# Optimization experiments

Measured on AMD Instinct MI355X. Metric: run time of the kernel, lower is better.

Reference implementation:

```python
import jax, jax.numpy as jnp
import numpy as np

REMOVE_FACTOR = 1000000.0


def setup_inputs() -> dict:
    key = jax.random.key(0)
    ks = jax.random.split(key, 6)
    B, Te, Td = 4, 512, 128
    D_en, D_de, U = 256, 512, 128
    en_seq = jax.random.normal(ks[0], (B, Te, D_en), dtype=jnp.float32)
    de_seq = jax.random.normal(ks[1], (B, Td, D_de), dtype=jnp.float32)
    mask = jax.random.randint(ks[2], (B, Te), 0, 2).astype(jnp.int32)
    w_en = jax.random.normal(ks[3], (D_en, U), dtype=jnp.float32) * (1.0 / np.sqrt(D_en))
    w_de = jax.random.normal(ks[4], (D_de, U), dtype=jnp.float32) * (1.0 / np.sqrt(D_de))
    nu = jax.random.normal(ks[5], (U, 1), dtype=jnp.float32) * (1.0 / np.sqrt(U))
    return {"en_seq": en_seq, "de_seq": de_seq, "mask": mask,
            "w_en": w_en, "w_de": w_de, "nu": nu}


def reference(en_seq, de_seq, mask, w_en, w_de, nu):
    # en_seq: [B,Te,D_en], de_seq: [B,Td,D_de], mask: [B,Te] (0/1)
    m = mask.astype(en_seq.dtype)
    en = en_seq * m[..., None]                         # masked encoder states
    en_p = jnp.einsum('bte,eu->btu', en, w_en)          # [B,Te,U]
    de_p = jnp.einsum('bdf,fu->bdu', de_seq, w_de)      # [B,Td,U]
    # additive (Bahdanau) scores: scores[b,td,te] = tanh(en_p[te]+de_p[td]) @ nu
    h = jnp.tanh(en_p[:, None, :, :] + de_p[:, :, None, :])  # [B,Td,Te,U]
    mu = jnp.einsum('bdtu,u->bdt', h, nu[:, 0])               # [B,Td,Te]
    mu = mu + (m[:, None, :] - 1.0) * REMOVE_FACTOR           # mask bias
    alphas = jax.nn.softmax(mu, axis=-1)                      # softmax over Te
    sum_en = jnp.einsum('bdt,btc->bdc', alphas, en)           # [B,Td,D_en]
    return jnp.concatenate([de_seq, sum_en], axis=-1)         # [B,Td,D_de+D_en]
```

## Files before the change

### kernel.cpp

```cpp
#include <hip/hip_runtime.h>

namespace {
constexpr int B = 4, Te = 512, Td = 128, Den = 256, Dde = 512, U = 128;
constexpr float REMOVE = 1000000.0f;
constexpr float L2E2 = 2.885390081777927f;

__device__ __forceinline__ unsigned short f2bf(float f) {
  unsigned u = __float_as_uint(f);
  u += 0x7FFFu + ((u >> 16) & 1u);
  return (unsigned short)(u >> 16);
}
__device__ __forceinline__ float bf2f(unsigned short h) {
  return __uint_as_float(((unsigned)h) << 16);
}
__device__ __forceinline__ void tanh_fma(float ep, float dv, float nv, float& acc) {
  float e = __builtin_amdgcn_exp2f((ep + dv) * L2E2);
  float r = __builtin_amdgcn_rcpf(e + 1.0f);
  acc = fmaf(fmaf(-2.0f, r, 1.0f), nv, acc);
}
__device__ __forceinline__ void fma4(const float4& w, float x, float* a) {
  a[0] = fmaf(x, w.x, a[0]); a[1] = fmaf(x, w.y, a[1]);
  a[2] = fmaf(x, w.z, a[2]); a[3] = fmaf(x, w.w, a[3]);
}

__global__ __launch_bounds__(512) void proj_kernel(
    const float* __restrict__ en_seq, const float* __restrict__ de_seq,
    const int* __restrict__ mask, const float* __restrict__ w_en,
    const float* __restrict__ w_de, unsigned short* __restrict__ en_pT,
    unsigned short* __restrict__ en_bf, float* __restrict__ de_pA,
    float* __restrict__ de_pB, float* __restrict__ out) {
  __shared__ float xs[4096];
  const int blk = blockIdx.x, tid = threadIdx.x;

  if (blk < 128) {
    const int r0 = blk * 16;
    for (int i = tid; i < 1024; i += 512) {
      int row = i >> 6, c4 = i & 63;
      float m = (float)mask[r0 + row];
      float4 v = *(const float4*)(en_seq + (size_t)(r0 + row) * Den + c4 * 4);
      v.x *= m; v.y *= m; v.z *= m; v.w *= m;
      *(float4*)(xs + row * 256 + c4 * 4) = v;
      ushort4 h; h.x = f2bf(v.x); h.y = f2bf(v.y); h.z = f2bf(v.z); h.w = f2bf(v.w);
      *(ushort4*)(en_bf + (size_t)(r0 + row) * Den + c4 * 4) = h;
    }
    __syncthreads();
    const int rg = tid >> 5, ug = tid & 31, u0 = ug * 4;
    float acc[4] = {0, 0, 0, 0};
    for (int k = 0; k < 256; k += 4) {
      const float* wp = w_en + (size_t)k * U + u0;
      float4 w0 = *(const float4*)(wp);
      float4 w1 = *(const float4*)(wp + U);
      float4 w2 = *(const float4*)(wp + 2 * U);
      float4 w3 = *(const float4*)(wp + 3 * U);
      float4 xv = *(const float4*)(xs + rg * 256 + k);
      fma4(w0, xv.x, acc); fma4(w1, xv.y, acc);
      fma4(w2, xv.z, acc); fma4(w3, xv.w, acc);
    }
    __syncthreads();
#pragma unroll
    for (int j = 0; j < 4; ++j) xs[(u0 + j) * 17 + rg] = acc[j];
    __syncthreads();
    {
      int u = tid >> 2, q = tid & 3;
      const float* p = xs + u * 17 + q * 4;
      ushort4 h; h.x = f2bf(p[0]); h.y = f2bf(p[1]); h.z = f2bf(p[2]); h.w = f2bf(p[3]);
      int b = r0 >> 9, teb = (r0 & 511) + q * 4;
      *(ushort4*)(en_pT + ((size_t)b * U + u) * Te + teb) = h;
    }
  } else {
    const int q = blk - 128, rt = q >> 1, kh = q & 1;
    const int r0 = rt * 8, k0 = kh * 256;
    {
      int row = tid >> 6, c4 = tid & 63;
      float4 v = *(const float4*)(de_seq + (size_t)(r0 + row) * Dde + k0 + c4 * 4);
      *(float4*)(xs + row * 256 + c4 * 4) = v;
      *(float4*)(out + (size_t)(r0 + row) * 768 + k0 + c4 * 4) = v;
    }
    __syncthreads();
    const int ks = tid >> 8, rg = (tid >> 5) & 7, ug = tid & 31, u0 = ug * 4;
    float acc[4] = {0, 0, 0, 0};
    for (int k = ks * 128; k < ks * 128 + 128; k += 4) {
      const float* wp = w_de + (size_t)(k0 + k) * U + u0;
      float4 w0 = *(const float4*)(wp);
      float4 w1 = *(const float4*)(wp + U);
      float4 w2 = *(const float4*)(wp + 2 * U);
      float4 w3 = *(const float4*)(wp + 3 * U);
      float4 xv = *(const float4*)(xs + rg * 256 + k);
      fma4(w0, xv.x, acc); fma4(w1, xv.y, acc);
      fma4(w2, xv.z, acc); fma4(w3, xv.w, acc);
    }
    __syncthreads();
    *(float4*)(xs + (ks * 8 + rg) * 128 + u0) =
        make_float4(acc[0], acc[1], acc[2], acc[3]);
    __syncthreads();
    float* dst = kh ? de_pB : de_pA;
    for (int i = tid; i < 1024; i += 512) {
      int r = i >> 7, u = i & 127;
      dst[(size_t)(r0 + r) * U + u] = xs[r * 128 + u] + xs[(8 + r) * 128 + u];
    }
  }
}

__global__ __launch_bounds__(512) void attn_kernel(
    const unsigned short* __restrict__ en_pT, const unsigned short* __restrict__ en_bf,
    const float* __restrict__ de_pA, const float* __restrict__ de_pB,
    const float* __restrict__ nu, const int* __restrict__ mask,
    float* __restrict__ out) {
  __shared__ float dep[256];
  __shared__ float nus[128];
  __shared__ float mbs[512];
  __shared__ float als[1024];
  __shared__ float scr[4096];
  const int blk = blockIdx.x, tid = threadIdx.x;
  const int b = blk >> 6, tp = blk & 63;
  const int gtd0 = b * Td + tp * 2;

  mbs[tid] = ((float)mask[b * Te + tid] - 1.0f) * REMOVE;
  if (tid < 64) {
    int r = tid >> 5, q = tid & 31;
    float4 a = *(const float4*)(de_pA + (size_t)(gtd0 + r) * U + q * 4);
    float4 c = *(const float4*)(de_pB + (size_t)(gtd0 + r) * U + q * 4);
    *(float4*)(dep + r * 128 + q * 4) =
        make_float4(a.x + c.x, a.y + c.y, a.z + c.z, a.w + c.w);
  } else if (tid < 96) {
    int q2 = tid - 64;
    *(float4*)(nus + q2 * 4) = *(const float4*)(nu + q2 * 4);
  }
  __syncthreads();

  {
    const int ts = tid & 127, uq = tid >> 7;
    const int te0 = ts * 4;
    float s0[4] = {0, 0, 0, 0}, s1[4] = {0, 0, 0, 0};
    const unsigned short* ep = en_pT + (size_t)b * U * Te;
#pragma unroll 4
    for (int u = uq * 32; u < uq * 32 + 32; ++u) {
      ushort4 h = *(const ushort4*)(ep + (size_t)u * Te + te0);
      float dv0 = dep[u], dv1 = dep[128 + u], nv = nus[u];
      float e0 = bf2f(h.x), e1 = bf2f(h.y), e2 = bf2f(h.z), e3 = bf2f(h.w);
      tanh_fma(e0, dv0, nv, s0[0]); tanh_fma(e0, dv1, nv, s1[0]);
      tanh_fma(e1, dv0, nv, s0[1]); tanh_fma(e1, dv1, nv, s1[1]);
      tanh_fma(e2, dv0, nv, s0[2]); tanh_fma(e2, dv1, nv, s1[2]);
      tanh_fma(e3, dv0, nv, s0[3]); tanh_fma(e3, dv1, nv, s1[3]);
    }
    *(float4*)(scr + (uq * 2 + 0) * 512 + te0) = make_float4(s0[0], s0[1], s0[2], s0[3]);
    *(float4*)(scr + (uq * 2 + 1) * 512 + te0) = make_float4(s1[0], s1[1], s1[2], s1[3]);
  }
  __syncthreads();

  {
    const int wid = tid >> 6, lane = tid & 63;
    if (wid < 2) {
      float v[8]; float mx = -3.0e38f;
#pragma unroll
      for (int i = 0; i < 8; ++i) {
        int te = lane + i * 64;
        float s = scr[(0 + wid) * 512 + te] + scr[(2 + wid) * 512 + te] +
                  scr[(4 + wid) * 512 + te] + scr[(6 + wid) * 512 + te] + mbs[te];
        v[i] = s; mx = fmaxf(mx, s);
      }
#pragma unroll
      for (int o = 32; o >= 1; o >>= 1) mx = fmaxf(mx, __shfl_xor(mx, o));
      float ssum = 0.f;
#pragma unroll
      for (int i = 0; i < 8; ++i) { v[i] = __expf(v[i] - mx); ssum += v[i]; }
#pragma unroll
      for (int o = 32; o >= 1; o >>= 1) ssum += __shfl_xor(ssum, o);
      float inv = 1.0f / ssum;
#pragma unroll
      for (int i = 0; i < 8; ++i) als[(lane + i * 64) * 2 + wid] = v[i] * inv;
    }
  }
  __syncthreads();

  {
    const int wid = tid >> 6, lane = tid & 63;
    const int ch0 = lane * 4;
    const unsigned short* eb = en_bf + (size_t)b * Te * Den;
    float p0[4] = {0, 0, 0, 0}, p1[4] = {0, 0, 0, 0};
#pragma unroll 4
    for (int t = 0; t < 64; ++t) {
      int te = wid * 64 + t;
      ushort4 h = *(const ushort4*)(eb + (size_t)te * Den + ch0);
      float2 al = *(const float2*)(als + te * 2);
      float e0 = bf2f(h.x), e1 = bf2f(h.y), e2 = bf2f(h.z), e3 = bf2f(h.w);
      p0[0] = fmaf(al.x, e0, p0[0]); p0[1] = fmaf(al.x, e1, p0[1]);
      p0[2] = fmaf(al.x, e2, p0[2]); p0[3] = fmaf(al.x, e3, p0[3]);
      p1[0] = fmaf(al.y, e0, p1[0]); p1[1] = fmaf(al.y, e1, p1[1]);
      p1[2] = fmaf(al.y, e2, p1[2]); p1[3] = fmaf(al.y, e3, p1[3]);
    }
    *(float4*)(scr + (wid * 2 + 0) * 256 + ch0) = make_float4(p0[0], p0[1], p0[2], p0[3]);
    *(float4*)(scr + (wid * 2 + 1) * 256 + ch0) = make_float4(p1[0], p1[1], p1[2], p1[3]);
  }
  __syncthreads();

  {
    int td = tid >> 8, ch = tid & 255;
    float v = 0.f;
#pragma unroll
    for (int w = 0; w < 8; ++w) v += scr[(w * 2 + td) * 256 + ch];
    out[(size_t)(gtd0 + td) * 768 + 512 + ch] = v;
  }
}
}

extern "C" void kernel_launch(void* const* d_in, const int* in_sizes, int n_in,
                              void* d_out, int out_size, void* d_ws, size_t ws_size,
                              hipStream_t stream) {
  const float* en_seq = (const float*)d_in[0];
  const float* de_seq = (const float*)d_in[1];
  const int*   mask   = (const int*)d_in[2];
  const float* w_en   = (const float*)d_in[3];
  const float* w_de   = (const float*)d_in[4];
  const float* nu     = (const float*)d_in[5];
  float* out = (float*)d_out;

  unsigned short* en_pT = (unsigned short*)d_ws;
  unsigned short* en_bf = en_pT + (size_t)B * U * Te;
  float* de_pA = (float*)(en_bf + (size_t)B * Te * Den);
  float* de_pB = de_pA + (size_t)B * Td * U;

  hipLaunchKernelGGL(proj_kernel, dim3(256), dim3(512), 0, stream,
                     en_seq, de_seq, mask, w_en, w_de, en_pT, en_bf,
                     de_pA, de_pB, out);
  hipLaunchKernelGGL(attn_kernel, dim3(256), dim3(512), 0, stream,
                     en_pT, en_bf, de_pA, de_pB, nu, mask, out);
}
```

Baseline: 41.12 us.

## Repartition both kernels into smaller 256-thread blocks with one decoder row per block

Both kernels move from 512-thread to 256-thread blocks with more blocks each. The attention kernel now handles one decoder timestep per block instead of two, so the 64x8 softmax layout becomes a block-wide reduction through shared-memory warp partials. The projection kernel halves its rows per block and drops the split-K reduction through shared memory. The aim is more blocks to fill the CUs and less shared memory per block, but each en_pT and en_bf tile is now reread once per decoder row instead of shared across two, roughly doubling that traffic.

Measured after the change: 42.65 us. 1.04x slower.

```diff
diff --git a/kernel.cpp b/kernel.cpp
--- a/kernel.cpp
+++ b/kernel.cpp
@@ -23,18 +23,18 @@
   a[2] = fmaf(x, w.z, a[2]); a[3] = fmaf(x, w.w, a[3]);
 }
 
-__global__ __launch_bounds__(512) void proj_kernel(
+__global__ __launch_bounds__(256) void proj_kernel(
     const float* __restrict__ en_seq, const float* __restrict__ de_seq,
     const int* __restrict__ mask, const float* __restrict__ w_en,
     const float* __restrict__ w_de, unsigned short* __restrict__ en_pT,
     unsigned short* __restrict__ en_bf, float* __restrict__ de_pA,
     float* __restrict__ de_pB, float* __restrict__ out) {
-  __shared__ float xs[4096];
+  __shared__ float xs[2048];
   const int blk = blockIdx.x, tid = threadIdx.x;
 
-  if (blk < 128) {
-    const int r0 = blk * 16;
-    for (int i = tid; i < 1024; i += 512) {
+  if (blk < 256) {
+    const int r0 = blk * 8;
+    for (int i = tid; i < 512; i += 256) {
       int row = i >> 6, c4 = i & 63;
       float m = (float)mask[r0 + row];
       float4 v = *(const float4*)(en_seq + (size_t)(r0 + row) * Den + c4 * 4);
@@ -46,6 +46,7 @@
     __syncthreads();
     const int rg = tid >> 5, ug = tid & 31, u0 = ug * 4;
     float acc[4] = {0, 0, 0, 0};
+#pragma unroll 4
     for (int k = 0; k < 256; k += 4) {
       const float* wp = w_en + (size_t)k * U + u0;
       float4 w0 = *(const float4*)(wp);
@@ -57,29 +58,34 @@
       fma4(w2, xv.z, acc); fma4(w3, xv.w, acc);
     }
     __syncthreads();
-#pragma unroll
-    for (int j = 0; j < 4; ++j) xs[(u0 + j) * 17 + rg] = acc[j];
-    __syncthreads();
-    {
-      int u = tid >> 2, q = tid & 3;
-      const float* p = xs + u * 17 + q * 4;
-      ushort4 h; h.x = f2bf(p[0]); h.y = f2bf(p[1]); h.z = f2bf(p[2]); h.w = f2bf(p[3]);
-      int b = r0 >> 9, teb = (r0 & 511) + q * 4;
-      *(ushort4*)(en_pT + ((size_t)b * U + u) * Te + teb) = h;
+    *(float4*)(xs + rg * 128 + u0) = make_float4(acc[0], acc[1], acc[2], acc[3]);
+    __syncthreads();
+    if (tid < 128) {
+      int u = tid;
+      int b = r0 >> 9, te0 = r0 & 511;
+      ushort4 h0, h1;
+      h0.x = f2bf(xs[0 * 128 + u]); h0.y = f2bf(xs[1 * 128 + u]);
+      h0.z = f2bf(xs[2 * 128 + u]); h0.w = f2bf(xs[3 * 128 + u]);
+      h1.x = f2bf(xs[4 * 128 + u]); h1.y = f2bf(xs[5 * 128 + u]);
+      h1.z = f2bf(xs[6 * 128 + u]); h1.w = f2bf(xs[7 * 128 + u]);
+      unsigned short* dst = en_pT + ((size_t)b * U + u) * Te + te0;
+      *(ushort4*)(dst) = h0;
+      *(ushort4*)(dst + 4) = h1;
     }
   } else {
-    const int q = blk - 128, rt = q >> 1, kh = q & 1;
+    const int q = blk - 256, rt = q >> 1, kh = q & 1;
     const int r0 = rt * 8, k0 = kh * 256;
-    {
-      int row = tid >> 6, c4 = tid & 63;
+    for (int i = tid; i < 512; i += 256) {
+      int row = i >> 6, c4 = i & 63;
       float4 v = *(const float4*)(de_seq + (size_t)(r0 + row) * Dde + k0 + c4 * 4);
       *(float4*)(xs + row * 256 + c4 * 4) = v;
       *(float4*)(out + (size_t)(r0 + row) * 768 + k0 + c4 * 4) = v;
     }
     __syncthreads();
-    const int ks = tid >> 8, rg = (tid >> 5) & 7, ug = tid & 31, u0 = ug * 4;
+    const int rg = tid >> 5, ug = tid & 31, u0 = ug * 4;
     float acc[4] = {0, 0, 0, 0};
-    for (int k = ks * 128; k < ks * 128 + 128; k += 4) {
+#pragma unroll 4
+    for (int k = 0; k < 256; k += 4) {
       const float* wp = w_de + (size_t)(k0 + k) * U + u0;
       float4 w0 = *(const float4*)(wp);
       float4 w1 = *(const float4*)(wp + U);
@@ -89,41 +95,32 @@
       fma4(w0, xv.x, acc); fma4(w1, xv.y, acc);
       fma4(w2, xv.z, acc); fma4(w3, xv.w, acc);
     }
-    __syncthreads();
-    *(float4*)(xs + (ks * 8 + rg) * 128 + u0) =
+    float* dst = kh ? de_pB : de_pA;
+    *(float4*)(dst + (size_t)(r0 + rg) * U + u0) =
         make_float4(acc[0], acc[1], acc[2], acc[3]);
-    __syncthreads();
-    float* dst = kh ? de_pB : de_pA;
-    for (int i = tid; i < 1024; i += 512) {
-      int r = i >> 7, u = i & 127;
-      dst[(size_t)(r0 + r) * U + u] = xs[r * 128 + u] + xs[(8 + r) * 128 + u];
-    }
-  }
-}
-
-__global__ __launch_bounds__(512) void attn_kernel(
+  }
+}
+
+__global__ __launch_bounds__(256) void attn_kernel(
     const unsigned short* __restrict__ en_pT, const unsigned short* __restrict__ en_bf,
     const float* __restrict__ de_pA, const float* __restrict__ de_pB,
     const float* __restrict__ nu, const int* __restrict__ mask,
     float* __restrict__ out) {
-  __shared__ float dep[256];
-  __shared__ float nus[128];
-  __shared__ float mbs[512];
-  __shared__ float als[1024];
-  __shared__ float scr[4096];
+  __shared__ float dep[128], nus[128], mbs[512], als[512];
+  __shared__ float scr[1024];
+  __shared__ float wredA[4], wredB[4];
   const int blk = blockIdx.x, tid = threadIdx.x;
-  const int b = blk >> 6, tp = blk & 63;
-  const int gtd0 = b * Td + tp * 2;
-
-  mbs[tid] = ((float)mask[b * Te + tid] - 1.0f) * REMOVE;
-  if (tid < 64) {
-    int r = tid >> 5, q = tid & 31;
-    float4 a = *(const float4*)(de_pA + (size_t)(gtd0 + r) * U + q * 4);
-    float4 c = *(const float4*)(de_pB + (size_t)(gtd0 + r) * U + q * 4);
-    *(float4*)(dep + r * 128 + q * 4) =
+  const int b = blk >> 7, gtd = blk;
+
+  mbs[tid]       = ((float)mask[b * Te + tid] - 1.0f) * REMOVE;
+  mbs[tid + 256] = ((float)mask[b * Te + tid + 256] - 1.0f) * REMOVE;
+  if (tid < 32) {
+    float4 a = *(const float4*)(de_pA + (size_t)gtd * U + tid * 4);
+    float4 c = *(const float4*)(de_pB + (size_t)gtd * U + tid * 4);
+    *(float4*)(dep + tid * 4) =
         make_float4(a.x + c.x, a.y + c.y, a.z + c.z, a.w + c.w);
-  } else if (tid < 96) {
-    int q2 = tid - 64;
+  } else if (tid < 64) {
+    int q2 = tid - 32;
     *(float4*)(nus + q2 * 4) = *(const float4*)(nu + q2 * 4);
   }
   __syncthreads();
@@ -131,76 +128,62 @@
   {
     const int ts = tid & 127, uq = tid >> 7;
     const int te0 = ts * 4;
-    float s0[4] = {0, 0, 0, 0}, s1[4] = {0, 0, 0, 0};
     const unsigned short* ep = en_pT + (size_t)b * U * Te;
-#pragma unroll 4
-    for (int u = uq * 32; u < uq * 32 + 32; ++u) {
+    float s[4] = {0, 0, 0, 0};
+#pragma unroll 8
+    for (int u = uq * 64; u < uq * 64 + 64; ++u) {
       ushort4 h = *(const ushort4*)(ep + (size_t)u * Te + te0);
-      float dv0 = dep[u], dv1 = dep[128 + u], nv = nus[u];
-      float e0 = bf2f(h.x), e1 = bf2f(h.y), e2 = bf2f(h.z), e3 = bf2f(h.w);
-      tanh_fma(e0, dv0, nv, s0[0]); tanh_fma(e0, dv1, nv, s1[0]);
-      tanh_fma(e1, dv0, nv, s0[1]); tanh_fma(e1, dv1, nv, s1[1]);
-      tanh_fma(e2, dv0, nv, s0[2]); tanh_fma(e2, dv1, nv, s1[2]);
-      tanh_fma(e3, dv0, nv, s0[3]); tanh_fma(e3, dv1, nv, s1[3]);
-    }
-    *(float4*)(scr + (uq * 2 + 0) * 512 + te0) = make_float4(s0[0], s0[1], s0[2], s0[3]);
-    *(float4*)(scr + (uq * 2 + 1) * 512 + te0) = make_float4(s1[0], s1[1], s1[2], s1[3]);
+      float dv = dep[u], nv = nus[u];
+      tanh_fma(bf2f(h.x), dv, nv, s[0]);
+      tanh_fma(bf2f(h.y), dv, nv, s[1]);
+      tanh_fma(bf2f(h.z), dv, nv, s[2]);
+      tanh_fma(bf2f(h.w), dv, nv, s[3]);
+    }
+    *(float4*)(scr + uq * 512 + te0) = make_float4(s[0], s[1], s[2], s[3]);
   }
   __syncthreads();
 
   {
-    const int wid = tid >> 6, lane = tid & 63;
-    if (wid < 2) {
-      float v[8]; float mx = -3.0e38f;
+    const int wid = tid >> 6;
+    float v0 = scr[tid] + scr[512 + tid] + mbs[tid];
+    float v1 = scr[tid + 256] + scr[512 + tid + 256] + mbs[tid + 256];
+    float mx = fmaxf(v0, v1);
 #pragma unroll
-      for (int i = 0; i < 8; ++i) {
-        int te = lane + i * 64;
-        float s = scr[(0 + wid) * 512 + te] + scr[(2 + wid) * 512 + te] +
-                  scr[(4 + wid) * 512 + te] + scr[(6 + wid) * 512 + te] + mbs[te];
-        v[i] = s; mx = fmaxf(mx, s);
-      }
+    for (int o = 32; o >= 1; o >>= 1) mx = fmaxf(mx, __shfl_xor(mx, o));
+    if ((tid & 63) == 0) wredA[wid] = mx;
+    __syncthreads();
+    float bm = fmaxf(fmaxf(wredA[0], wredA[1]), fmaxf(wredA[2], wredA[3]));
+    float e0 = __expf(v0 - bm), e1 = __expf(v1 - bm);
+    float ss = e0 + e1;
 #pragma unroll
-      for (int o = 32; o >= 1; o >>= 1) mx = fmaxf(mx, __shfl_xor(mx, o));
-      float ssum = 0.f;
-#pragma unroll
-      for (int i = 0; i < 8; ++i) { v[i] = __expf(v[i] - mx); ssum += v[i]; }
-#pragma unroll
-      for (int o = 32; o >= 1; o >>= 1) ssum += __shfl_xor(ssum, o);
-      float inv = 1.0f / ssum;
-#pragma unroll
-      for (int i = 0; i < 8; ++i) als[(lane + i * 64) * 2 + wid] = v[i] * inv;
-    }
+    for (int o = 32; o >= 1; o >>= 1) ss += __shfl_xor(ss, o);
+    if ((tid & 63) == 0) wredB[wid] = ss;
+    __syncthreads();
+    float inv = 1.0f / (wredB[0] + wredB[1] + wredB[2] + wredB[3]);
+    als[tid] = e0 * inv;
+    als[tid + 256] = e1 * inv;
   }
   __syncthreads();
 
   {
-    const int wid = tid >> 6, lane = tid & 63;
-    const int ch0 = lane * 4;
+    const int cq = tid & 63, teq = tid >> 6;
+    const int c0 = cq * 4;
     const unsigned short* eb = en_bf + (size_t)b * Te * Den;
-    float p0[4] = {0, 0, 0, 0}, p1[4] = {0, 0, 0, 0};
-#pragma unroll 4
-    for (int t = 0; t < 64; ++t) {
-      int te = wid * 64 + t;
-      ushort4 h = *(const ushort4*)(eb + (size_t)te * Den + ch0);
-      float2 al = *(const float2*)(als + te * 2);
-      float e0 = bf2f(h.x), e1 = bf2f(h.y), e2 = bf2f(h.z), e3 = bf2f(h.w);
-      p0[0] = fmaf(al.x, e0, p0[0]); p0[1] = fmaf(al.x, e1, p0[1]);
-      p0[2] = fmaf(al.x, e2, p0[2]); p0[3] = fmaf(al.x, e3, p0[3]);
-      p1[0] = fmaf(al.y, e0, p1[0]); p1[1] = fmaf(al.y, e1, p1[1]);
-      p1[2] = fmaf(al.y, e2, p1[2]); p1[3] = fmaf(al.y, e3, p1[3]);
-    }
-    *(float4*)(scr + (wid * 2 + 0) * 256 + ch0) = make_float4(p0[0], p0[1], p0[2], p0[3]);
-    *(float4*)(scr + (wid * 2 + 1) * 256 + ch0) = make_float4(p1[0], p1[1], p1[2], p1[3]);
-  }
-  __syncthreads();
-
-  {
-    int td = tid >> 8, ch = tid & 255;
-    float v = 0.f;
-#pragma unroll
-    for (int w = 0; w < 8; ++w) v += scr[(w * 2 + td) * 256 + ch];
-    out[(size_t)(gtd0 + td) * 768 + 512 + ch] = v;
-  }
+    float p[4] = {0, 0, 0, 0};
+#pragma unroll 8
+    for (int t = 0; t < 128; ++t) {
+      int te = teq * 128 + t;
+      ushort4 h = *(const ushort4*)(eb + (size_t)te * Den + c0);
+      float al = als[te];
+      p[0] = fmaf(al, bf2f(h.x), p[0]); p[1] = fmaf(al, bf2f(h.y), p[1]);
+      p[2] = fmaf(al, bf2f(h.z), p[2]); p[3] = fmaf(al, bf2f(h.w), p[3]);
+    }
+    *(float4*)(scr + teq * 256 + c0) = make_float4(p[0], p[1], p[2], p[3]);
+  }
+  __syncthreads();
+
+  out[(size_t)gtd * 768 + 512 + tid] =
+      scr[tid] + scr[256 + tid] + scr[512 + tid] + scr[768 + tid];
 }
 }
 
@@ -220,9 +203,9 @@
   float* de_pA = (float*)(en_bf + (size_t)B * Te * Den);
   float* de_pB = de_pA + (size_t)B * Td * U;
 
-  hipLaunchKernelGGL(proj_kernel, dim3(256), dim3(512), 0, stream,
+  hipLaunchKernelGGL(proj_kernel, dim3(384), dim3(256), 0, stream,
                      en_seq, de_seq, mask, w_en, w_de, en_pT, en_bf,
                      de_pA, de_pB, out);
-  hipLaunchKernelGGL(attn_kernel, dim3(256), dim3(512), 0, stream,
+  hipLaunchKernelGGL(attn_kernel, dim3(512), dim3(256), 0, stream,
                      en_pT, en_bf, de_pA, de_pB, nu, mask, out);
 }
```

## Split attention into score and output kernels with tiled LDS score computation

Applied to the files above, without the earlier changes.

Replaces the fused attention kernel with a score kernel and a separate softmax/weighted-sum kernel. The score kernel stages a 64×128 tile of en_p into swizzled LDS and computes 8 decoder rows per block across 512 blocks. Scores go to a global mu buffer. en_p is stored row-major in te-tiles instead of transposed. The projection kernel is retuned to 256 threads with wider per-thread accumulators. This aims to raise parallelism and reuse in the tanh-heavy score phase, at the cost of an extra launch and a global round trip for the scores.

Result: no change. 41.01 us (-0.3%).

```diff
diff --git a/kernel.cpp b/kernel.cpp
--- a/kernel.cpp
+++ b/kernel.cpp
@@ -23,7 +23,7 @@
   a[2] = fmaf(x, w.z, a[2]); a[3] = fmaf(x, w.w, a[3]);
 }
 
-__global__ __launch_bounds__(512) void proj_kernel(
+__global__ __launch_bounds__(256) void proj_kernel(
     const float* __restrict__ en_seq, const float* __restrict__ de_seq,
     const int* __restrict__ mask, const float* __restrict__ w_en,
     const float* __restrict__ w_de, unsigned short* __restrict__ en_pT,
@@ -34,7 +34,7 @@
 
   if (blk < 128) {
     const int r0 = blk * 16;
-    for (int i = tid; i < 1024; i += 512) {
+    for (int i = tid; i < 1024; i += 256) {
       int row = i >> 6, c4 = i & 63;
       float m = (float)mask[r0 + row];
       float4 v = *(const float4*)(en_seq + (size_t)(r0 + row) * Den + c4 * 4);
@@ -44,42 +44,51 @@
       *(ushort4*)(en_bf + (size_t)(r0 + row) * Den + c4 * 4) = h;
     }
     __syncthreads();
-    const int rg = tid >> 5, ug = tid & 31, u0 = ug * 4;
-    float acc[4] = {0, 0, 0, 0};
+    const int rg = tid >> 4, ug = tid & 15, u0 = ug * 8;
+    float acc[8] = {0, 0, 0, 0, 0, 0, 0, 0};
+#pragma unroll 2
     for (int k = 0; k < 256; k += 4) {
       const float* wp = w_en + (size_t)k * U + u0;
-      float4 w0 = *(const float4*)(wp);
-      float4 w1 = *(const float4*)(wp + U);
-      float4 w2 = *(const float4*)(wp + 2 * U);
-      float4 w3 = *(const float4*)(wp + 3 * U);
+      float4 wa0 = *(const float4*)(wp),         wb0 = *(const float4*)(wp + 4);
+      float4 wa1 = *(const float4*)(wp + U),     wb1 = *(const float4*)(wp + U + 4);
+      float4 wa2 = *(const float4*)(wp + 2 * U), wb2 = *(const float4*)(wp + 2 * U + 4);
+      float4 wa3 = *(const float4*)(wp + 3 * U), wb3 = *(const float4*)(wp + 3 * U + 4);
       float4 xv = *(const float4*)(xs + rg * 256 + k);
-      fma4(w0, xv.x, acc); fma4(w1, xv.y, acc);
-      fma4(w2, xv.z, acc); fma4(w3, xv.w, acc);
-    }
-    __syncthreads();
-#pragma unroll
-    for (int j = 0; j < 4; ++j) xs[(u0 + j) * 17 + rg] = acc[j];
+      fma4(wa0, xv.x, acc); fma4(wb0, xv.x, acc + 4);
+      fma4(wa1, xv.y, acc); fma4(wb1, xv.y, acc + 4);
+      fma4(wa2, xv.z, acc); fma4(wb2, xv.z, acc + 4);
+      fma4(wa3, xv.w, acc); fma4(wb3, xv.w, acc + 4);
+    }
+    __syncthreads();
+    *(float4*)(xs + rg * 128 + u0)     = make_float4(acc[0], acc[1], acc[2], acc[3]);
+    *(float4*)(xs + rg * 128 + u0 + 4) = make_float4(acc[4], acc[5], acc[6], acc[7]);
     __syncthreads();
     {
-      int u = tid >> 2, q = tid & 3;
-      const float* p = xs + u * 17 + q * 4;
-      ushort4 h; h.x = f2bf(p[0]); h.y = f2bf(p[1]); h.z = f2bf(p[2]); h.w = f2bf(p[3]);
-      int b = r0 >> 9, teb = (r0 & 511) + q * 4;
-      *(ushort4*)(en_pT + ((size_t)b * U + u) * Te + teb) = h;
+      int r = tid >> 4, uo = (tid & 15) * 8;
+      const float* p = xs + r * 128 + uo;
+      ushort4 h0, h1;
+      h0.x = f2bf(p[0]); h0.y = f2bf(p[1]); h0.z = f2bf(p[2]); h0.w = f2bf(p[3]);
+      h1.x = f2bf(p[4]); h1.y = f2bf(p[5]); h1.z = f2bf(p[6]); h1.w = f2bf(p[7]);
+      int b = r0 >> 9, teT = (r0 >> 6) & 7, tein0 = r0 & 63;
+      unsigned short* dst =
+          en_pT + ((size_t)(b * 8 + teT) * 64 + tein0 + r) * U + uo;
+      *(ushort4*)dst = h0;
+      *(ushort4*)(dst + 4) = h1;
     }
   } else {
     const int q = blk - 128, rt = q >> 1, kh = q & 1;
     const int r0 = rt * 8, k0 = kh * 256;
-    {
-      int row = tid >> 6, c4 = tid & 63;
+    for (int i = tid; i < 512; i += 256) {
+      int row = i >> 6, c4 = i & 63;
       float4 v = *(const float4*)(de_seq + (size_t)(r0 + row) * Dde + k0 + c4 * 4);
       *(float4*)(xs + row * 256 + c4 * 4) = v;
       *(float4*)(out + (size_t)(r0 + row) * 768 + k0 + c4 * 4) = v;
     }
     __syncthreads();
-    const int ks = tid >> 8, rg = (tid >> 5) & 7, ug = tid & 31, u0 = ug * 4;
+    const int rg = tid >> 5, ug = tid & 31, u0 = ug * 4;
     float acc[4] = {0, 0, 0, 0};
-    for (int k = ks * 128; k < ks * 128 + 128; k += 4) {
+#pragma unroll 4
+    for (int k = 0; k < 256; k += 4) {
       const float* wp = w_de + (size_t)(k0 + k) * U + u0;
       float4 w0 = *(const float4*)(wp);
       float4 w1 = *(const float4*)(wp + U);
@@ -89,117 +98,128 @@
       fma4(w0, xv.x, acc); fma4(w1, xv.y, acc);
       fma4(w2, xv.z, acc); fma4(w3, xv.w, acc);
     }
-    __syncthreads();
-    *(float4*)(xs + (ks * 8 + rg) * 128 + u0) =
+    float* dst = kh ? de_pB : de_pA;
+    *(float4*)(dst + (size_t)(r0 + rg) * U + u0) =
         make_float4(acc[0], acc[1], acc[2], acc[3]);
-    __syncthreads();
-    float* dst = kh ? de_pB : de_pA;
-    for (int i = tid; i < 1024; i += 512) {
-      int r = i >> 7, u = i & 127;
-      dst[(size_t)(r0 + r) * U + u] = xs[r * 128 + u] + xs[(8 + r) * 128 + u];
-    }
-  }
-}
-
-__global__ __launch_bounds__(512) void attn_kernel(
-    const unsigned short* __restrict__ en_pT, const unsigned short* __restrict__ en_bf,
-    const float* __restrict__ de_pA, const float* __restrict__ de_pB,
-    const float* __restrict__ nu, const int* __restrict__ mask,
-    float* __restrict__ out) {
-  __shared__ float dep[256];
+  }
+}
+
+__global__ __launch_bounds__(256) void score_kernel(
+    const unsigned short* __restrict__ en_pT, const float* __restrict__ de_pA,
+    const float* __restrict__ de_pB, const float* __restrict__ nu,
+    const int* __restrict__ mask, float* __restrict__ mu) {
+  __shared__ float tile[64 * 128];
+  __shared__ float dep[8 * 128];
   __shared__ float nus[128];
-  __shared__ float mbs[512];
-  __shared__ float als[1024];
-  __shared__ float scr[4096];
   const int blk = blockIdx.x, tid = threadIdx.x;
-  const int b = blk >> 6, tp = blk & 63;
-  const int gtd0 = b * Td + tp * 2;
-
-  mbs[tid] = ((float)mask[b * Te + tid] - 1.0f) * REMOVE;
-  if (tid < 64) {
-    int r = tid >> 5, q = tid & 31;
-    float4 a = *(const float4*)(de_pA + (size_t)(gtd0 + r) * U + q * 4);
-    float4 c = *(const float4*)(de_pB + (size_t)(gtd0 + r) * U + q * 4);
-    *(float4*)(dep + r * 128 + q * 4) =
+  const int teT = blk & 7, tdT = (blk >> 3) & 15, b = blk >> 7;
+  const int te0 = teT * 64, td0 = tdT * 8;
+
+  const unsigned short* src = en_pT + (size_t)(b * 8 + teT) * 64 * U;
+#pragma unroll
+  for (int j = 0; j < 4; ++j) {
+    int unit = j * 256 + tid;
+    int te = unit >> 4, u0 = (unit & 15) * 8;
+    ushort4 ha = *(const ushort4*)(src + (size_t)te * U + u0);
+    ushort4 hb = *(const ushort4*)(src + (size_t)te * U + u0 + 4);
+    int sw = te & 31;
+    float4 f0 = make_float4(bf2f(ha.x), bf2f(ha.y), bf2f(ha.z), bf2f(ha.w));
+    float4 f1 = make_float4(bf2f(hb.x), bf2f(hb.y), bf2f(hb.z), bf2f(hb.w));
+    *(float4*)(tile + te * 128 + (((u0 >> 2) + 0) ^ sw) * 4) = f0;
+    *(float4*)(tile + te * 128 + (((u0 >> 2) + 1) ^ sw) * 4) = f1;
+  }
+  {
+    int row = tid >> 5, qq = tid & 31;
+    float4 a = *(const float4*)(de_pA + (size_t)(b * Td + td0 + row) * U + qq * 4);
+    float4 c = *(const float4*)(de_pB + (size_t)(b * Td + td0 + row) * U + qq * 4);
+    *(float4*)(dep + row * 128 + qq * 4) =
         make_float4(a.x + c.x, a.y + c.y, a.z + c.z, a.w + c.w);
-  } else if (tid < 96) {
-    int q2 = tid - 64;
-    *(float4*)(nus + q2 * 4) = *(const float4*)(nu + q2 * 4);
+    if (tid < 32) *(float4*)(nus + tid * 4) = *(const float4*)(nu + tid * 4);
   }
   __syncthreads();
 
+  const int te = tid & 63, tdq = tid >> 6, sw = te & 31;
+  const float4* trow = (const float4*)(tile + te * 128);
+  const float* d0 = dep + (tdq * 2 + 0) * 128;
+  const float* d1 = dep + (tdq * 2 + 1) * 128;
+  float s0 = 0.f, s1 = 0.f;
+#pragma unroll 4
+  for (int q = 0; q < 32; ++q) {
+    float4 ev = trow[q ^ sw];
+    float4 av = *(const float4*)(d0 + q * 4);
+    float4 bv = *(const float4*)(d1 + q * 4);
+    float4 nv = *(const float4*)(nus + q * 4);
+    tanh_fma(ev.x, av.x, nv.x, s0); tanh_fma(ev.x, bv.x, nv.x, s1);
+    tanh_fma(ev.y, av.y, nv.y, s0); tanh_fma(ev.y, bv.y, nv.y, s1);
+    tanh_fma(ev.z, av.z, nv.z, s0); tanh_fma(ev.z, bv.z, nv.z, s1);
+    tanh_fma(ev.w, av.w, nv.w, s0); tanh_fma(ev.w, bv.w, nv.w, s1);
+  }
+  const int gte = te0 + te;
+  float bias = ((float)mask[b * Te + gte] - 1.0f) * REMOVE;
+  mu[(size_t)(b * Td + td0 + tdq * 2 + 0) * Te + gte] = s0 + bias;
+  mu[(size_t)(b * Td + td0 + tdq * 2 + 1) * Te + gte] = s1 + bias;
+}
+
+__global__ __launch_bounds__(512) void out_kernel(
+    const unsigned short* __restrict__ en_bf, const int* __restrict__ mask,
+    const float* __restrict__ mu, float* __restrict__ out) {
+  __shared__ float al[Te * 4];
+  __shared__ float part[8 * 4 * 128];
+  const int blk = blockIdx.x, tid = threadIdx.x;
+  const int chH = blk & 1, tdT = (blk >> 1) & 31, b = blk >> 6;
+  const int td0 = tdT * 4;
+  const int wid = tid >> 6, lane = tid & 63;
+
+  if (wid < 4) {
+    const float* murow = mu + (size_t)(b * Td + td0 + wid) * Te;
+    const int* mrow = mask + b * Te;
+    float v[8]; float mx = -3.0e38f;
+#pragma unroll
+    for (int i = 0; i < 8; ++i) { v[i] = murow[lane + i * 64]; mx = fmaxf(mx, v[i]); }
+#pragma unroll
+    for (int o = 32; o >= 1; o >>= 1) mx = fmaxf(mx, __shfl_xor(mx, o));
+    float ss = 0.f;
+#pragma unroll
+    for (int i = 0; i < 8; ++i) { v[i] = __expf(v[i] - mx); ss += v[i]; }
+#pragma unroll
+    for (int o = 32; o >= 1; o >>= 1) ss += __shfl_xor(ss, o);
+    float inv = 1.0f / ss;
+#pragma unroll
+    for (int i = 0; i < 8; ++i) {
+      int te = lane + i * 64;
+      al[te * 4 + wid] = v[i] * inv * (float)mrow[te];
+    }
+  }
+  __syncthreads();
+
   {
-    const int ts = tid & 127, uq = tid >> 7;
-    const int te0 = ts * 4;
-    float s0[4] = {0, 0, 0, 0}, s1[4] = {0, 0, 0, 0};
-    const unsigned short* ep = en_pT + (size_t)b * U * Te;
-#pragma unroll 4
-    for (int u = uq * 32; u < uq * 32 + 32; ++u) {
-      ushort4 h = *(const ushort4*)(ep + (size_t)u * Te + te0);
-      float dv0 = dep[u], dv1 = dep[128 + u], nv = nus[u];
-      float e0 = bf2f(h.x), e1 = bf2f(h.y), e2 = bf2f(h.z), e3 = bf2f(h.w);
-      tanh_fma(e0, dv0, nv, s0[0]); tanh_fma(e0, dv1, nv, s1[0]);
-      tanh_fma(e1, dv0, nv, s0[1]); tanh_fma(e1, dv1, nv, s1[1]);
-      tanh_fma(e2, dv0, nv, s0[2]); tanh_fma(e2, dv1, nv, s1[2]);
-      tanh_fma(e3, dv0, nv, s0[3]); tanh_fma(e3, dv1, nv, s1[3]);
-    }
-    *(float4*)(scr + (uq * 2 + 0) * 512 + te0) = make_float4(s0[0], s0[1], s0[2], s0[3]);
-    *(float4*)(scr + (uq * 2 + 1) * 512 + te0) = make_float4(s1[0], s1[1], s1[2], s1[3]);
-  }
-  __syncthreads();
-
-  {
-    const int wid = tid >> 6, lane = tid & 63;
-    if (wid < 2) {
-      float v[8]; float mx = -3.0e38f;
-#pragma unroll
-      for (int i = 0; i < 8; ++i) {
-        int te = lane + i * 64;
-        float s = scr[(0 + wid) * 512 + te] + scr[(2 + wid) * 512 + te] +
-                  scr[(4 + wid) * 512 + te] + scr[(6 + wid) * 512 + te] + mbs[te];
-        v[i] = s; mx = fmaxf(mx, s);
-      }
-#pragma unroll
-      for (int o = 32; o >= 1; o >>= 1) mx = fmaxf(mx, __shfl_xor(mx, o));
-      float ssum = 0.f;
-#pragma unroll
-      for (int i = 0; i < 8; ++i) { v[i] = __expf(v[i] - mx); ssum += v[i]; }
-#pragma unroll
-      for (int o = 32; o >= 1; o >>= 1) ssum += __shfl_xor(ssum, o);
-      float inv = 1.0f / ssum;
-#pragma unroll
-      for (int i = 0; i < 8; ++i) als[(lane + i * 64) * 2 + wid] = v[i] * inv;
-    }
-  }
-  __syncthreads();
-
-  {
-    const int wid = tid >> 6, lane = tid & 63;
-    const int ch0 = lane * 4;
-    const unsigned short* eb = en_bf + (size_t)b * Te * Den;
-    float p0[4] = {0, 0, 0, 0}, p1[4] = {0, 0, 0, 0};
+    const int c0 = chH * 128 + lane * 2;
+    const unsigned short* eb = en_bf + (size_t)b * Te * Den + c0;
+    float a00 = 0, a01 = 0, a10 = 0, a11 = 0, a20 = 0, a21 = 0, a30 = 0, a31 = 0;
 #pragma unroll 4
     for (int t = 0; t < 64; ++t) {
       int te = wid * 64 + t;
-      ushort4 h = *(const ushort4*)(eb + (size_t)te * Den + ch0);
-      float2 al = *(const float2*)(als + te * 2);
-      float e0 = bf2f(h.x), e1 = bf2f(h.y), e2 = bf2f(h.z), e3 = bf2f(h.w);
-      p0[0] = fmaf(al.x, e0, p0[0]); p0[1] = fmaf(al.x, e1, p0[1]);
-      p0[2] = fmaf(al.x, e2, p0[2]); p0[3] = fmaf(al.x, e3, p0[3]);
-      p1[0] = fmaf(al.y, e0, p1[0]); p1[1] = fmaf(al.y, e1, p1[1]);
-      p1[2] = fmaf(al.y, e2, p1[2]); p1[3] = fmaf(al.y, e3, p1[3]);
-    }
-    *(float4*)(scr + (wid * 2 + 0) * 256 + ch0) = make_float4(p0[0], p0[1], p0[2], p0[3]);
-    *(float4*)(scr + (wid * 2 + 1) * 256 + ch0) = make_float4(p1[0], p1[1], p1[2], p1[3]);
+      ushort2 h = *(const ushort2*)(eb + (size_t)te * Den);
+      float4 av = *(const float4*)(al + te * 4);
+      float e0 = bf2f(h.x), e1 = bf2f(h.y);
+      a00 = fmaf(av.x, e0, a00); a01 = fmaf(av.x, e1, a01);
+      a10 = fmaf(av.y, e0, a10); a11 = fmaf(av.y, e1, a11);
+      a20 = fmaf(av.z, e0, a20); a21 = fmaf(av.z, e1, a21);
+      a30 = fmaf(av.w, e0, a30); a31 = fmaf(av.w, e1, a31);
+    }
+    *(float2*)(part + (wid * 4 + 0) * 128 + lane * 2) = make_float2(a00, a01);
+    *(float2*)(part + (wid * 4 + 1) * 128 + lane * 2) = make_float2(a10, a11);
+    *(float2*)(part + (wid * 4 + 2) * 128 + lane * 2) = make_float2(a20, a21);
+    *(float2*)(part + (wid * 4 + 3) * 128 + lane * 2) = make_float2(a30, a31);
   }
   __syncthreads();
 
   {
-    int td = tid >> 8, ch = tid & 255;
-    float v = 0.f;
-#pragma unroll
-    for (int w = 0; w < 8; ++w) v += scr[(w * 2 + td) * 256 + ch];
-    out[(size_t)(gtd0 + td) * 768 + 512 + ch] = v;
+    int td = tid >> 7, cc = tid & 127;
+    float r = 0.f;
+#pragma unroll
+    for (int w = 0; w < 8; ++w) r += part[(w * 4 + td) * 128 + cc];
+    out[(size_t)(b * Td + td0 + td) * 768 + 512 + chH * 128 + cc] = r;
   }
 }
 }
@@ -216,13 +236,16 @@
   float* out = (float*)d_out;
 
   unsigned short* en_pT = (unsigned short*)d_ws;
-  unsigned short* en_bf = en_pT + (size_t)B * U * Te;
+  unsigned short* en_bf = en_pT + (size_t)B * Te * U;
   float* de_pA = (float*)(en_bf + (size_t)B * Te * Den);
   float* de_pB = de_pA + (size_t)B * Td * U;
-
-  hipLaunchKernelGGL(proj_kernel, dim3(256), dim3(512), 0, stream,
+  float* mu    = de_pB + (size_t)B * Td * U;
+
+  hipLaunchKernelGGL(proj_kernel, dim3(256), dim3(256), 0, stream,
                      en_seq, de_seq, mask, w_en, w_de, en_pT, en_bf,
                      de_pA, de_pB, out);
-  hipLaunchKernelGGL(attn_kernel, dim3(256), dim3(512), 0, stream,
-                     en_pT, en_bf, de_pA, de_pB, nu, mask, out);
-}
+  hipLaunchKernelGGL(score_kernel, dim3(512), dim3(256), 0, stream,
+                     en_pT, de_pA, de_pB, nu, mask, mu);
+  hipLaunchKernelGGL(out_kernel, dim3(256), dim3(512), 0, stream,
+                     en_bf, mask, mu, out);
+}
```
